# Kernel tuning notes

Hardware: AMD Instinct MI355X
Metric: run time of the kernel (lower is better)

Reference implementation:

```python
import jax, jax.numpy as jnp
import numpy as np

H = W = 128          # image_size
K = 8                # faces_per_pixel
EPS = 1e-8
BIG = 1e10           # sentinel z for non-covering faces


def _rasterize(vertices, faces):
    # vertices: (B, V, 3) NDC x,y (+x left, +y up, pytorch3d convention), camera z > 0
    # faces:    (B, F, 3) int indices into V
    fv = jax.vmap(lambda v, f: v[f])(vertices, faces)  # (B, F, 3, 3)
    vx, vy, vz = fv[..., 0], fv[..., 1], fv[..., 2]     # (B, F, 3)

    def e(a):
        return a[:, None, None, :]                      # (B, 1, 1, F)

    x0, x1, x2 = e(vx[..., 0]), e(vx[..., 1]), e(vx[..., 2])
    y0, y1, y2 = e(vy[..., 0]), e(vy[..., 1]), e(vy[..., 2])
    z0, z1, z2 = e(vz[..., 0]), e(vz[..., 1]), e(vz[..., 2])

    dt = vertices.dtype
    PX = (1.0 - 2.0 * (jnp.arange(W, dtype=dt) + 0.5) / W)[None, None, :, None]  # (1,1,W,1)
    PY = (1.0 - 2.0 * (jnp.arange(H, dtype=dt) + 0.5) / H)[None, :, None, None]  # (1,H,1,1)

    def edge_fn(ax, ay, bx, by):
        # signed area of (a, b, pixel); broadcasts to (B, H, W, F)
        return (bx - ax) * (PY - ay) - (by - ay) * (PX - ax)

    w0 = edge_fn(x1, y1, x2, y2)
    w1 = edge_fn(x2, y2, x0, y0)
    w2 = edge_fn(x0, y0, x1, y1)
    area = (x1 - x0) * (y2 - y0) - (y1 - y0) * (x2 - x0)       # (B,1,1,F)
    area_safe = jnp.where(jnp.abs(area) < EPS, EPS, area)

    # screen-space barycentrics
    b0 = w0 / area_safe
    b1 = w1 / area_safe
    b2 = w2 / area_safe
    inside = (b0 >= 0) & (b1 >= 0) & (b2 >= 0) & (jnp.abs(area) > EPS)

    # perspective-correct barycentrics (pytorch3d barycentric_perspective_correct)
    n0 = b0 * z1 * z2
    n1 = z0 * b1 * z2
    n2 = z0 * z1 * b2
    den = n0 + n1 + n2
    den_safe = jnp.where(jnp.abs(den) < EPS, EPS, den)
    p0 = n0 / den_safe
    p1 = n1 / den_safe
    p2 = n2 / den_safe

    zpix = p0 * z0 + p1 * z1 + p2 * z2                          # (B,H,W,F)
    zs = jnp.where(inside, zpix, BIG)

    # per-pixel nearest-K z-buffer over all faces
    negz, idx = jax.lax.top_k(-zs, K)                           # (B,H,W,K)
    zbuf = -negz
    valid = zbuf < 0.5 * BIG
    pix_to_face = jnp.where(valid, idx, -1)

    g = lambda a: jnp.take_along_axis(a, idx, axis=-1)
    bary = jnp.stack([g(p0), g(p1), g(p2)], axis=-1)            # (B,H,W,K,3)
    bary = jnp.where(valid[..., None], bary, -1.0)
    zbuf = jnp.where(valid, zbuf, -1.0)

    # signed squared NDC distance of pixel to nearest triangle edge (negative inside)
    def edge_d2(ax, ay, bx, by):
        ex = bx - ax
        ey = by - ay
        l2 = jnp.maximum(ex * ex + ey * ey, EPS)
        t = jnp.clip(((PX - ax) * ex + (PY - ay) * ey) / l2, 0.0, 1.0)
        dx = PX - (ax + t * ex)
        dy = PY - (ay + t * ey)
        return dx * dx + dy * dy

    d2 = jnp.minimum(edge_d2(x0, y0, x1, y1),
                     jnp.minimum(edge_d2(x1, y1, x2, y2), edge_d2(x2, y2, x0, y0)))
    sd = jnp.where(inside, -d2, d2)
    dists = jnp.where(valid, g(sd), -1.0)                       # (B,H,W,K)

    return pix_to_face, zbuf, bary, dists


def setup_inputs() -> dict:
    key = jax.random.key(0)
    k1, k2, k3 = jax.random.split(key, 3)
    B, V, F = 1, 600, 1000
    xy = jax.random.uniform(k1, (B, V, 2), minval=-1.0, maxval=1.0)
    z = jax.random.uniform(k2, (B, V, 1), minval=1.0, maxval=3.0)
    vertices = jnp.concatenate([xy, z], axis=-1)
    faces = jax.random.randint(k3, (B, F, 3), 0, V)
    return {"vertices": vertices, "faces": faces}


def reference(vertices, faces):
    # Fragments: (pix_to_face, zbuf, bary_coords, dists)
    return _rasterize(vertices, faces)
```

## Files before the change

kernel.cpp:

```cpp
#include <hip/hip_runtime.h>


#define HW_    128
#define KF     8
#define NPIX   (HW_ * HW_)
#define EPSf   1e-8f
#define BIGf   1e10f
#define SCAP   512
#define BBMARG 1e-4f
#define EDGEM  1e-3f

typedef unsigned long long ull;

#define CE(X, Y) { ull _mn = (X) < (Y) ? (X) : (Y); ull _mx = (X) < (Y) ? (Y) : (X); (X) = _mn; (Y) = _mx; }

__device__ __forceinline__ float edge_d2_fn(float px, float py,
                                            float ax, float ay,
                                            float bx, float by) {
#pragma clang fp contract(off)
    float ex = bx - ax;
    float ey = by - ay;
    float l2 = fmaxf(ex * ex + ey * ey, EPSf);
    float t  = ((px - ax) * ex + (py - ay) * ey) / l2;
    t = fminf(fmaxf(t, 0.0f), 1.0f);
    float dx = px - (ax + t * ex);
    float dy = py - (ay + t * ey);
    return dx * dx + dy * dy;
}

__device__ __forceinline__ bool tile_keep(
    float x0, float y0, float x1, float y1, float x2, float y2, float area,
    float pxlo, float pxhi, float pylo, float pyhi)
{
#pragma clang fp contract(off)
    float xmn = fminf(x0, fminf(x1, x2)) - BBMARG;
    float xmx = fmaxf(x0, fmaxf(x1, x2)) + BBMARG;
    float ymn = fminf(y0, fminf(y1, y2)) - BBMARG;
    float ymx = fmaxf(y0, fmaxf(y1, y2)) + BBMARG;
    if (!((xmn <= pxhi) && (xmx >= pxlo) && (ymn <= pyhi) && (ymx >= pylo)))
        return false;
    float s = (area > 0.0f) ? 1.0f : -1.0f;
    float B0 = s * (x2 - x1), C0 = -s * (y2 - y1);
    float A0 = s * ((y2 - y1) * x1 - (x2 - x1) * y1);
    float B1 = s * (x0 - x2), C1 = -s * (y0 - y2);
    float A1 = s * ((y0 - y2) * x2 - (x0 - x2) * y2);
    float B2 = s * (x1 - x0), C2 = -s * (y1 - y0);
    float A2 = s * ((y1 - y0) * x0 - (x1 - x0) * y0);
    float w0m = A0 + fmaxf(B0 * pylo, B0 * pyhi) + fmaxf(C0 * pxlo, C0 * pxhi);
    float w1m = A1 + fmaxf(B1 * pylo, B1 * pyhi) + fmaxf(C1 * pxlo, C1 * pxhi);
    float w2m = A2 + fmaxf(B2 * pylo, B2 * pyhi) + fmaxf(C2 * pxlo, C2 * pxhi);
    return (w0m >= -EDGEM) && (w1m >= -EDGEM) && (w2m >= -EDGEM);
}

__global__ __launch_bounds__(512, 8) void raster_kernel(
    const float* __restrict__ verts,
    const int* __restrict__ faces,
    float* __restrict__ out,
    int F, int NV3)
{
#pragma clang fp contract(off)
    __shared__ __align__(16) char smem[31872];
    float4*   ga   = (float4*)smem;
    float4*   gb   = (float4*)(smem + 8192);
    float4*   gzf  = (float4*)(smem + 16384);
    unsigned* wtot = (unsigned*)(smem + 24576);
    float*    vlds = (float*)(smem + 24640);

    int tid  = threadIdx.x;
    int tile = blockIdx.x;
    int txi = tile & 31, tyi = tile >> 5;

    for (int i = tid; i < NV3; i += 512) vlds[i] = verts[i];

    float pxhi = 1.0f - (2.0f * ((float)(txi * 4)     + 0.5f)) / 128.0f;
    float pxlo = 1.0f - (2.0f * ((float)(txi * 4 + 3) + 0.5f)) / 128.0f;
    float pyhi = 1.0f - (2.0f * ((float)(tyi * 4)     + 0.5f)) / 128.0f;
    float pylo = 1.0f - (2.0f * ((float)(tyi * 4 + 3) + 0.5f)) / 128.0f;

    int lane = tid & 63;
    int wv   = tid >> 6;
    ull lmask = (1ull << lane) - 1ull;

    int fA = tid;
    int fB = tid + 512;
    bool vA = fA < F;
    bool vB = fB < F;
    int fAc = vA ? fA : 0;
    int fBc = vB ? fB : 0;
    int iA0 = faces[3 * fAc + 0], iA1 = faces[3 * fAc + 1], iA2 = faces[3 * fAc + 2];
    int iB0 = faces[3 * fBc + 0], iB1 = faces[3 * fBc + 1], iB2 = faces[3 * fBc + 2];

    __syncthreads();

    float ax0 = vlds[3 * iA0 + 0], ay0 = vlds[3 * iA0 + 1], az0 = vlds[3 * iA0 + 2];
    float ax1 = vlds[3 * iA1 + 0], ay1 = vlds[3 * iA1 + 1], az1 = vlds[3 * iA1 + 2];
    float ax2 = vlds[3 * iA2 + 0], ay2 = vlds[3 * iA2 + 1], az2 = vlds[3 * iA2 + 2];
    float areaA = (ax1 - ax0) * (ay2 - ay0) - (ay1 - ay0) * (ax2 - ax0);
    bool keepA = vA && tile_keep(ax0, ay0, ax1, ay1, ax2, ay2, areaA,
                                 pxlo, pxhi, pylo, pyhi);
    ull balA = __ballot(keepA);
    int belowA = __popcll(balA & lmask);

    float bx0 = vlds[3 * iB0 + 0], by0 = vlds[3 * iB0 + 1], bz0 = vlds[3 * iB0 + 2];
    float bx1 = vlds[3 * iB1 + 0], by1 = vlds[3 * iB1 + 1], bz1 = vlds[3 * iB1 + 2];
    float bx2 = vlds[3 * iB2 + 0], by2 = vlds[3 * iB2 + 1], bz2 = vlds[3 * iB2 + 2];
    float areaB = (bx1 - bx0) * (by2 - by0) - (by1 - by0) * (bx2 - bx0);
    bool keepB = vB && tile_keep(bx0, by0, bx1, by1, bx2, by2, areaB,
                                 pxlo, pxhi, pylo, pyhi);
    ull balB = __ballot(keepB);
    int belowB = __popcll(balB & lmask);

    if (lane == 0) {
        wtot[wv]     = (unsigned)__popcll(balA);
        wtot[8 + wv] = (unsigned)__popcll(balB);
    }
    __syncthreads();
    int preA = 0, totA = 0, preB = 0, totB = 0;
#pragma unroll
    for (int i = 0; i < 8; ++i) {
        int tA = (int)wtot[i], tB = (int)wtot[8 + i];
        if (i < wv) { preA += tA; preB += tB; }
        totA += tA; totB += tB;
    }
    int S = totA + totB;
    if (S > SCAP) S = SCAP;
    if (keepA) {
        int pos = preA + belowA;
        if (pos < SCAP) {
            ga[pos]  = make_float4(ax0, ay0, ax1, ay1);
            gb[pos]  = make_float4(ax2, ay2, az0, az1);
            gzf[pos] = make_float4(az2, areaA, (float)fA, 0.0f);
        }
    }
    if (keepB) {
        int pos = totA + preB + belowB;
        if (pos < SCAP) {
            ga[pos]  = make_float4(bx0, by0, bx1, by1);
            gb[pos]  = make_float4(bx2, by2, bz0, bz1);
            gzf[pos] = make_float4(bz2, areaB, (float)fB, 0.0f);
        }
    }
    __syncthreads();

    int p_ = (wv << 1) | (lane >> 5);
    int c  = lane & 31;
    int w = txi * 4 + (p_ & 3);
    int h = tyi * 4 + (p_ >> 2);
    float px = 1.0f - (2.0f * ((float)w + 0.5f)) / 128.0f;
    float py = 1.0f - (2.0f * ((float)h + 0.5f)) / 128.0f;

    const ull SENT = ((ull)0x501502F9u << 32) | 0xFFFFFFFFull;
    ull tk[KF];
#pragma unroll
    for (int k = 0; k < KF; ++k) tk[k] = SENT;

    int j0 = (S * c) >> 5;
    int j1 = (S * (c + 1)) >> 5;
    for (int j = j0; j < j1; ++j) {
        float4 A  = ga[j];
        float4 Bv = gb[j];
        float4 Zf = gzf[j];
        float x0 = A.x,  y0 = A.y,  x1 = A.z,  y1 = A.w;
        float x2 = Bv.x, y2 = Bv.y, z0 = Bv.z, z1 = Bv.w;
        float z2 = Zf.x, area = Zf.y;

        float w0 = (x2 - x1) * (py - y1) - (y2 - y1) * (px - x1);
        float w1 = (x0 - x2) * (py - y2) - (y0 - y2) * (px - x2);
        float w2 = (x1 - x0) * (py - y0) - (y1 - y0) * (px - x0);
        float aabs = fabsf(area);
        float s = (area > 0.0f) ? 1.0f : -1.0f;
        if (!(w0 * s >= 0.0f && w1 * s >= 0.0f && w2 * s >= 0.0f && aabs > EPSf))
            continue;

        float b0 = w0 / area;
        float b1 = w1 / area;
        float b2 = w2 / area;
        float n0 = b0 * z1 * z2;
        float n1 = z0 * b1 * z2;
        float n2 = z0 * z1 * b2;
        float den = n0 + n1 + n2;
        float dabs = fabsf(den);
        float den_safe = (dabs < EPSf) ? EPSf : den;
        float p0 = n0 / den_safe;
        float p1 = n1 / den_safe;
        float p2 = n2 / den_safe;
        float z = p0 * z0 + p1 * z1 + p2 * z2;

        ull key = ((ull)__float_as_uint(z) << 32) | (ull)(unsigned)j;
        if (key < tk[KF - 1]) {
            tk[KF - 1] = key;
#pragma unroll
            for (int k = KF - 1; k > 0; --k) CE(tk[k - 1], tk[k]);
        }
    }

#pragma unroll
    for (int d = 1; d < 32; d <<= 1) {
        ull cc[KF];
#pragma unroll
        for (int i = 0; i < KF; ++i) {
            ull bv = (ull)__shfl_xor((long long)tk[KF - 1 - i], d, 64);
            cc[i] = tk[i] < bv ? tk[i] : bv;
        }
        CE(cc[0], cc[4]); CE(cc[1], cc[5]); CE(cc[2], cc[6]); CE(cc[3], cc[7]);
        CE(cc[0], cc[2]); CE(cc[1], cc[3]); CE(cc[4], cc[6]); CE(cc[5], cc[7]);
        CE(cc[0], cc[1]); CE(cc[2], cc[3]); CE(cc[4], cc[5]); CE(cc[6], cc[7]);
#pragma unroll
        for (int i = 0; i < KF; ++i) tk[i] = cc[i];
    }

    int sub = lane & 31;
    ull key = tk[0];
#pragma unroll
    for (int k = 1; k < KF; ++k) key = (sub == k) ? tk[k] : key;

    if (sub < KF) {
        int k = sub;
        unsigned ju = (unsigned)(key & 0xFFFFFFFFULL);
        float zk = __uint_as_float((unsigned)(key >> 32));
        int base = (h * HW_ + w) * KF;

        float vp = -1.0f, vz = -1.0f, vb0 = -1.0f, vb1 = -1.0f, vb2 = -1.0f, vd = -1.0f;
        if (ju != 0xFFFFFFFFu && zk < 0.5f * BIGf) {
            int j = (int)ju;
            float4 A4 = ga[j];
            float4 B4 = gb[j];
            float4 Z4 = gzf[j];
            float x0 = A4.x, y0 = A4.y, x1 = A4.z, y1 = A4.w;
            float x2 = B4.x, y2 = B4.y, z0 = B4.z, z1 = B4.w;
            float z2 = Z4.x, area = Z4.y;
            float w0 = (x2 - x1) * (py - y1) - (y2 - y1) * (px - x1);
            float w1 = (x0 - x2) * (py - y2) - (y0 - y2) * (px - x2);
            float w2 = (x1 - x0) * (py - y0) - (y1 - y0) * (px - x0);
            float aabs = fabsf(area);
            float area_safe = (aabs < EPSf) ? EPSf : area;
            float b0 = w0 / area_safe;
            float b1 = w1 / area_safe;
            float b2 = w2 / area_safe;
            float n0 = b0 * z1 * z2;
            float n1 = z0 * b1 * z2;
            float n2 = z0 * z1 * b2;
            float den = n0 + n1 + n2;
            float dabs = fabsf(den);
            float den_safe = (dabs < EPSf) ? EPSf : den;
            float p0 = n0 / den_safe;
            float p1 = n1 / den_safe;
            float p2 = n2 / den_safe;
            float e0 = edge_d2_fn(px, py, x0, y0, x1, y1);
            float e1 = edge_d2_fn(px, py, x1, y1, x2, y2);
            float e2 = edge_d2_fn(px, py, x2, y2, x0, y0);
            float d2 = fminf(e0, fminf(e1, e2));
            vp = Z4.z;
            vz = zk;
            vb0 = p0; vb1 = p1; vb2 = p2;
            vd = -d2;
        }

        float* o_pix = out;
        float* o_z   = out + NPIX * KF;
        float* o_b   = out + 2 * NPIX * KF;
        float* o_d   = out + 2 * NPIX * KF + NPIX * KF * 3;
        o_pix[base + k] = vp;
        o_z[base + k]   = vz;
        o_b[(base + k) * 3 + 0] = vb0;
        o_b[(base + k) * 3 + 1] = vb1;
        o_b[(base + k) * 3 + 2] = vb2;
        o_d[base + k]   = vd;
    }
}

extern "C" void kernel_launch(void* const* d_in, const int* in_sizes, int n_in,
                              void* d_out, int out_size, void* d_ws, size_t ws_size,
                              hipStream_t stream) {
    const float* verts = (const float*)d_in[0];
    const int* faces = (const int*)d_in[1];
    float* out = (float*)d_out;
    int F = in_sizes[1] / 3;
    int NV3 = in_sizes[0];
    raster_kernel<<<dim3(1024), dim3(512), 0, stream>>>(verts, faces, out, F, NV3);
}
```

Baseline: 81.35 us.

## Use 8x4 pixel tiles with 1024-thread blocks and one face per thread

Tiles grow from 4x4 to 8x4 pixels, blocks from 512 to 1024 threads, and the grid is halved. Each thread now culls one face instead of two, which removes the second face-binning pass, and each face list is shared by twice as many pixels. The cost is that larger tiles pass more faces through the cull, so the per-pixel loops get longer. The wave-count scan now covers 16 waves, and with F=1000 faces at or above index 1024 are no longer handled.

```diff
diff --git a/kernel.cpp b/kernel.cpp
--- a/kernel.cpp
+++ b/kernel.cpp
@@ -52,14 +52,14 @@
     return (w0m >= -EDGEM) && (w1m >= -EDGEM) && (w2m >= -EDGEM);
 }
 
-__global__ __launch_bounds__(512, 8) void raster_kernel(
+__global__ __launch_bounds__(1024, 8) void raster_kernel(
     const float* __restrict__ verts,
     const int* __restrict__ faces,
     float* __restrict__ out,
     int F, int NV3)
 {
 #pragma clang fp contract(off)
-    __shared__ __align__(16) char smem[31872];
+    __shared__ __align__(16) char smem[31840];
     float4*   ga   = (float4*)smem;
     float4*   gb   = (float4*)(smem + 8192);
     float4*   gzf  = (float4*)(smem + 16384);
@@ -68,12 +68,12 @@
 
     int tid  = threadIdx.x;
     int tile = blockIdx.x;
-    int txi = tile & 31, tyi = tile >> 5;
-
-    for (int i = tid; i < NV3; i += 512) vlds[i] = verts[i];
-
-    float pxhi = 1.0f - (2.0f * ((float)(txi * 4)     + 0.5f)) / 128.0f;
-    float pxlo = 1.0f - (2.0f * ((float)(txi * 4 + 3) + 0.5f)) / 128.0f;
+    int txi = tile & 15, tyi = tile >> 4;
+
+    for (int i = tid; i < NV3; i += 1024) vlds[i] = verts[i];
+
+    float pxhi = 1.0f - (2.0f * ((float)(txi * 8)     + 0.5f)) / 128.0f;
+    float pxlo = 1.0f - (2.0f * ((float)(txi * 8 + 7) + 0.5f)) / 128.0f;
     float pyhi = 1.0f - (2.0f * ((float)(tyi * 4)     + 0.5f)) / 128.0f;
     float pylo = 1.0f - (2.0f * ((float)(tyi * 4 + 3) + 0.5f)) / 128.0f;
 
@@ -82,13 +82,9 @@
     ull lmask = (1ull << lane) - 1ull;
 
     int fA = tid;
-    int fB = tid + 512;
     bool vA = fA < F;
-    bool vB = fB < F;
     int fAc = vA ? fA : 0;
-    int fBc = vB ? fB : 0;
     int iA0 = faces[3 * fAc + 0], iA1 = faces[3 * fAc + 1], iA2 = faces[3 * fAc + 2];
-    int iB0 = faces[3 * fBc + 0], iB1 = faces[3 * fBc + 1], iB2 = faces[3 * fBc + 2];
 
     __syncthreads();
 
@@ -100,29 +96,16 @@
                                  pxlo, pxhi, pylo, pyhi);
     ull balA = __ballot(keepA);
     int belowA = __popcll(balA & lmask);
-
-    float bx0 = vlds[3 * iB0 + 0], by0 = vlds[3 * iB0 + 1], bz0 = vlds[3 * iB0 + 2];
-    float bx1 = vlds[3 * iB1 + 0], by1 = vlds[3 * iB1 + 1], bz1 = vlds[3 * iB1 + 2];
-    float bx2 = vlds[3 * iB2 + 0], by2 = vlds[3 * iB2 + 1], bz2 = vlds[3 * iB2 + 2];
-    float areaB = (bx1 - bx0) * (by2 - by0) - (by1 - by0) * (bx2 - bx0);
-    bool keepB = vB && tile_keep(bx0, by0, bx1, by1, bx2, by2, areaB,
-                                 pxlo, pxhi, pylo, pyhi);
-    ull balB = __ballot(keepB);
-    int belowB = __popcll(balB & lmask);
-
-    if (lane == 0) {
-        wtot[wv]     = (unsigned)__popcll(balA);
-        wtot[8 + wv] = (unsigned)__popcll(balB);
-    }
+    if (lane == 0) wtot[wv] = (unsigned)__popcll(balA);
     __syncthreads();
-    int preA = 0, totA = 0, preB = 0, totB = 0;
-#pragma unroll
-    for (int i = 0; i < 8; ++i) {
-        int tA = (int)wtot[i], tB = (int)wtot[8 + i];
-        if (i < wv) { preA += tA; preB += tB; }
-        totA += tA; totB += tB;
-    }
-    int S = totA + totB;
+    int preA = 0, totA = 0;
+#pragma unroll
+    for (int i = 0; i < 16; ++i) {
+        int t = (int)wtot[i];
+        if (i < wv) preA += t;
+        totA += t;
+    }
+    int S = totA;
     if (S > SCAP) S = SCAP;
     if (keepA) {
         int pos = preA + belowA;
@@ -132,20 +115,12 @@
             gzf[pos] = make_float4(az2, areaA, (float)fA, 0.0f);
         }
     }
-    if (keepB) {
-        int pos = totA + preB + belowB;
-        if (pos < SCAP) {
-            ga[pos]  = make_float4(bx0, by0, bx1, by1);
-            gb[pos]  = make_float4(bx2, by2, bz0, bz1);
-            gzf[pos] = make_float4(bz2, areaB, (float)fB, 0.0f);
-        }
-    }
     __syncthreads();
 
     int p_ = (wv << 1) | (lane >> 5);
     int c  = lane & 31;
-    int w = txi * 4 + (p_ & 3);
-    int h = tyi * 4 + (p_ >> 2);
+    int w = txi * 8 + (p_ & 7);
+    int h = tyi * 4 + (p_ >> 3);
     float px = 1.0f - (2.0f * ((float)w + 0.5f)) / 128.0f;
     float py = 1.0f - (2.0f * ((float)h + 0.5f)) / 128.0f;
 
@@ -277,5 +252,5 @@
     float* out = (float*)d_out;
     int F = in_sizes[1] / 3;
     int NV3 = in_sizes[0];
-    raster_kernel<<<dim3(1024), dim3(512), 0, stream>>>(verts, faces, out, F, NV3);
-}
+    raster_kernel<<<dim3(512), dim3(1024), 0, stream>>>(verts, faces, out, F, NV3);
+}
```

After: 84.38 us. 1.04x slower.
